# Kernel optimization log

Measured on AMD Instinct MI355X. Metric: run time of the kernel, lower is better.

## Reference

```python
import jax, jax.numpy as jnp
import numpy as np

B, S, DIN, E, H, L, F, DOUT = 16, 1024, 64, 512, 8, 6, 2048, 2
DH = E // H
EPS = 1e-5

def _make_pe(n, d):
    # replicates PositionalEncoding buffer: pe[pos, 2i]=sin, pe[pos,2i+1]=cos
    pos = np.arange(n, dtype=np.float32)[:, None]
    div = np.exp(np.arange(0, d, 2, dtype=np.float32) * (-np.log(10000.0) / d))
    pe = np.zeros((n, d), dtype=np.float32)
    pe[:, 0::2] = np.sin(pos * div)
    pe[:, 1::2] = np.cos(pos * div)
    return pe

def _layernorm(x, g, b):
    m = jnp.mean(x, axis=-1, keepdims=True)
    v = jnp.mean((x - m) ** 2, axis=-1, keepdims=True)
    return (x - m) * jax.lax.rsqrt(v + EPS) * g + b

def setup_inputs() -> dict:
    key = jax.random.key(0)
    ks = iter(jax.random.split(key, 40))
    def xavier(k, shape):
        fan_in, fan_out = shape[-2], shape[-1]
        lim = np.sqrt(6.0 / (fan_in + fan_out)).astype(np.float32)
        return jax.random.uniform(k, shape, jnp.float32, -lim, lim)
    inp = {}
    inp['x'] = jax.random.normal(next(ks), (B, S, DIN), jnp.float32)
    inp['Win'] = xavier(next(ks), (DIN, E)); inp['b_in'] = jnp.zeros((E,), jnp.float32)
    # pe[:x.size(0)] with batch-first x -> slice first B positions, broadcast over seq
    inp['pe'] = jnp.asarray(_make_pe(B, E))[:, None, :]  # [B,1,E]
    inp['Wq'] = xavier(next(ks), (L, E, E)); inp['bq'] = jnp.zeros((L, E), jnp.float32)
    inp['Wk'] = xavier(next(ks), (L, E, E)); inp['bk'] = jnp.zeros((L, E), jnp.float32)
    inp['Wv'] = xavier(next(ks), (L, E, E)); inp['bv'] = jnp.zeros((L, E), jnp.float32)
    inp['Wo'] = xavier(next(ks), (L, E, E)); inp['bo'] = jnp.zeros((L, E), jnp.float32)
    inp['g1'] = jnp.ones((L, E), jnp.float32); inp['be1'] = jnp.zeros((L, E), jnp.float32)
    inp['W1'] = xavier(next(ks), (L, E, F)); inp['b1'] = jnp.zeros((L, F), jnp.float32)
    inp['W2'] = xavier(next(ks), (L, F, E)); inp['b2'] = jnp.zeros((L, E), jnp.float32)
    inp['g2'] = jnp.ones((L, E), jnp.float32); inp['be2'] = jnp.zeros((L, E), jnp.float32)
    inp['gf'] = jnp.ones((E,), jnp.float32); inp['bef'] = jnp.zeros((E,), jnp.float32)
    inp['Wout'] = xavier(next(ks), (E, DOUT)); inp['bout'] = jnp.zeros((DOUT,), jnp.float32)
    return inp

def reference(x, Win, b_in, pe, Wq, bq, Wk, bk, Wv, bv, Wo, bo,
              g1, be1, W1, b1, W2, b2, g2, be2, gf, bef, Wout, bout):
    scale = 1.0 / np.sqrt(DH).astype(np.float32)
    h = x @ Win + b_in + pe  # [B,S,E], pe broadcast over seq (replicates source bug)
    for i in range(L):
        resid = h
        q = (h @ Wq[i] + bq[i]).reshape(B, S, H, DH)
        k = (h @ Wk[i] + bk[i]).reshape(B, S, H, DH)
        v = (h @ Wv[i] + bv[i]).reshape(B, S, H, DH)
        scores = jnp.einsum('bqhd,bkhd->bhqk', q, k) * scale
        attn = jax.nn.softmax(scores, axis=-1)
        o = jnp.einsum('bhqk,bkhd->bqhd', attn, v).reshape(B, S, E)
        o = o @ Wo[i] + bo[i]
        a = _layernorm(o + resid, g1[i], be1[i])
        f = jax.nn.relu(a @ W1[i] + b1[i]) @ W2[i] + b2[i]
        h = _layernorm(f + a, g2[i], be2[i])
    out = _layernorm(h, gf, bef) @ Wout + bout
    return out
```

## Files before the change

kernel.cpp:

```cpp
#include <hip/hip_runtime.h>
#include <hip/hip_bf16.h>

typedef __bf16 bf16_t;
typedef __bf16 bf16x8 __attribute__((ext_vector_type(8)));
typedef __bf16 bf16x4 __attribute__((ext_vector_type(4)));
typedef float f32x4 __attribute__((ext_vector_type(4)));

#define B_ 16
#define S_ 1024
#define E_ 512
#define H_ 8
#define DH_ 64
#define L_ 6
#define F_ 2048
#define M_ (B_ * S_)

#define EXP2F(x) __builtin_amdgcn_exp2f(x)

#define GLOAD_LDS16(gsrc, ldst) \
    __builtin_amdgcn_global_load_lds((const __attribute__((address_space(1))) void*)(gsrc), \
                                     (__attribute__((address_space(3))) void*)(ldst), 16, 0, 0)

__global__ void cast_bf16_kernel(const float* __restrict__ src, bf16_t* __restrict__ dst, int n) {
    int i = (blockIdx.x * 256 + threadIdx.x) * 4;
    if (i + 3 < n) {
        f32x4 v = *(const f32x4*)&src[i];
        #pragma unroll
        for (int j = 0; j < 4; ++j) dst[i + j] = (bf16_t)v[j];
    }
}

__global__ void castT_kernel(const float* __restrict__ src, bf16_t* __restrict__ dst,
                             int K, int N, size_t dstZ) {
    __shared__ bf16_t tile[32][33];
    size_t so = (size_t)blockIdx.z * K * N;
    size_t dofs = (size_t)blockIdx.z * dstZ;
    int k0 = blockIdx.y * 32, n0 = blockIdx.x * 32;
    int tx = threadIdx.x, ty = threadIdx.y;
    for (int i = ty; i < 32; i += 8)
        tile[i][tx] = (bf16_t)src[so + (size_t)(k0 + i) * N + n0 + tx];
    __syncthreads();
    for (int i = ty; i < 32; i += 8)
        dst[dofs + (size_t)(n0 + i) * K + k0 + tx] = tile[tx][i];
}

__global__ void pack_bias_kernel(const float* __restrict__ bq, const float* __restrict__ bk,
                                 const float* __restrict__ bv, float* __restrict__ dst) {
    int i = blockIdx.x * 256 + threadIdx.x;
    if (i >= L_ * 1536) return;
    int l = i / 1536, c = i % 1536;
    float v = (c < 512) ? bq[l * 512 + c] : (c < 1024 ? bk[l * 512 + c - 512] : bv[l * 512 + c - 1024]);
    dst[i] = v;
}

template<int EPI, bool RELU>
__launch_bounds__(256, 2)
__global__ void gemm_kernel(const bf16_t* __restrict__ A, const bf16_t* __restrict__ BT,
                            const float* __restrict__ bias, bf16_t* __restrict__ out16,
                            const float* __restrict__ auxf,
                            int M, int N, int K)
{
    __shared__ bf16_t As[2][128][32];
    __shared__ bf16_t Bs[2][128][32];
    const int tid = threadIdx.x;
    const int lane = tid & 63;
    const int w = tid >> 6;
    const int wm = w >> 1, wn = w & 1;
    const int m0 = blockIdx.x * 128, n0 = blockIdx.y * 128;
    const int l15 = lane & 15, lg = lane >> 4;

    const int srow = w * 32 + (lane >> 2);
    const int scol = (lane & 3) * 8;
    const bf16_t* Ab = A + (size_t)(m0 + srow) * K + scol;
    const bf16_t* Bb = BT + (size_t)(n0 + srow) * K + scol;

    f32x4 acc[4][4] = {};
    const int nt = K >> 5;

    #define STAGE(buf, t) do { \
        size_t ko_ = (size_t)(t) * 32; \
        _Pragma("unroll") \
        for (int j_ = 0; j_ < 2; ++j_) { \
            GLOAD_LDS16(Ab + (size_t)j_ * 16 * K + ko_, &As[buf][w * 32 + j_ * 16][0]); \
            GLOAD_LDS16(Bb + (size_t)j_ * 16 * K + ko_, &Bs[buf][w * 32 + j_ * 16][0]); \
        } } while (0)

    STAGE(0, 0);
    __syncthreads();
    int cur = 0;
    for (int t = 0; t < nt; ++t) {
        if (t + 1 < nt) STAGE(cur ^ 1, t + 1);
        bf16x8 af[4], bfr[4];
        #pragma unroll
        for (int m = 0; m < 4; ++m) af[m] = *(const bf16x8*)&As[cur][wm * 64 + m * 16 + l15][lg * 8];
        #pragma unroll
        for (int n = 0; n < 4; ++n) bfr[n] = *(const bf16x8*)&Bs[cur][wn * 64 + n * 16 + l15][lg * 8];
        __builtin_amdgcn_s_setprio(1);
        #pragma unroll
        for (int m = 0; m < 4; ++m)
            #pragma unroll
            for (int n = 0; n < 4; ++n)
                acc[m][n] = __builtin_amdgcn_mfma_f32_16x16x32_bf16(af[m], bfr[n], acc[m][n], 0, 0, 0);
        __builtin_amdgcn_s_setprio(0);
        __syncthreads();
        cur ^= 1;
    }
    #undef STAGE

    #pragma unroll
    for (int m = 0; m < 4; ++m) {
        #pragma unroll
        for (int n = 0; n < 4; ++n) {
            int col = n0 + wn * 64 + n * 16 + l15;
            float bv = bias[col];
            #pragma unroll
            for (int r = 0; r < 4; ++r) {
                int row = m0 + wm * 64 + m * 16 + lg * 4 + r;
                float v = acc[m][n][r] + bv;
                if (EPI == 1) v += auxf[(size_t)(row >> 10) * E_ + col];
                if (RELU) v = fmaxf(v, 0.f);
                out16[(size_t)row * N + col] = (bf16_t)v;
            }
        }
    }
}

template<int EPI, bool RELU>
__launch_bounds__(512, 2)
__global__ void gemm2_kernel(const bf16_t* __restrict__ A, const bf16_t* __restrict__ BT,
                             const float* __restrict__ bias, bf16_t* __restrict__ out16,
                             const bf16_t* __restrict__ auxb,
                             bf16_t* __restrict__ outk, bf16_t* __restrict__ outv,
                             int M, int N, int K)
{
    __shared__ bf16_t AB[4][12288];
    const int tid = threadIdx.x;
    const int lane = tid & 63;
    const int w = tid >> 6;
    const int wr = w >> 2, wc = w & 3;
    const int m0 = blockIdx.x * 128, n0 = blockIdx.y * 256;
    const int l15 = lane & 15, lg = lane >> 4;

    const int srow = w * 16 + (lane >> 2);
    const int scol = ((lane & 3) ^ ((lane >> 3) & 3)) * 8;
    const int cswz = (lg ^ ((l15 >> 1) & 3)) * 8;
    const bf16_t* Ab  = A  + (size_t)(m0 + srow) * K + scol;
    const bf16_t* Bb0 = BT + (size_t)(n0 + srow) * K + scol;
    const bf16_t* Bb1 = BT + (size_t)(n0 + 128 + srow) * K + scol;

    f32x4 acc[4][4] = {};
    const int nt = K >> 5;

    #define STAGE3(kt, buf) do { \
        size_t ko_ = (size_t)(kt) * 32; \
        GLOAD_LDS16(Ab  + ko_, &AB[buf][w * 512]); \
        GLOAD_LDS16(Bb0 + ko_, &AB[buf][4096 + w * 512]); \
        GLOAD_LDS16(Bb1 + ko_, &AB[buf][8192 + w * 512]); \
    } while (0)

    STAGE3(0, 0);
    STAGE3(1, 1);
    asm volatile("s_waitcnt vmcnt(3)" ::: "memory");
    __builtin_amdgcn_s_barrier();

    int t = 0;
    for (; t + 2 < nt; ++t) {
        const int cur = t & 3;
        bf16x8 af[4], bf[4];
        #pragma unroll
        for (int m = 0; m < 4; ++m)
            af[m] = *(const bf16x8*)&AB[cur][(wr * 64 + m * 16 + l15) * 32 + cswz];
        #pragma unroll
        for (int n = 0; n < 4; ++n)
            bf[n] = *(const bf16x8*)&AB[cur][4096 + (wc * 64 + n * 16 + l15) * 32 + cswz];
        STAGE3(t + 2, (t + 2) & 3);
        asm volatile("s_waitcnt vmcnt(3)" ::: "memory");
        __builtin_amdgcn_s_barrier();
        __builtin_amdgcn_s_setprio(1);
        #pragma unroll
        for (int m = 0; m < 4; ++m)
            #pragma unroll
            for (int n = 0; n < 4; ++n)
                acc[m][n] = __builtin_amdgcn_mfma_f32_16x16x32_bf16(af[m], bf[n], acc[m][n], 0, 0, 0);
        __builtin_amdgcn_s_setprio(0);
    }
    for (; t < nt; ++t) {
        const int cur = t & 3;
        bf16x8 af[4], bf[4];
        #pragma unroll
        for (int m = 0; m < 4; ++m)
            af[m] = *(const bf16x8*)&AB[cur][(wr * 64 + m * 16 + l15) * 32 + cswz];
        #pragma unroll
        for (int n = 0; n < 4; ++n)
            bf[n] = *(const bf16x8*)&AB[cur][4096 + (wc * 64 + n * 16 + l15) * 32 + cswz];
        asm volatile("s_waitcnt vmcnt(0)" ::: "memory");
        __builtin_amdgcn_s_barrier();
        __builtin_amdgcn_s_setprio(1);
        #pragma unroll
        for (int m = 0; m < 4; ++m)
            #pragma unroll
            for (int n = 0; n < 4; ++n)
                acc[m][n] = __builtin_amdgcn_mfma_f32_16x16x32_bf16(af[m], bf[n], acc[m][n], 0, 0, 0);
        __builtin_amdgcn_s_setprio(0);
    }
    #undef STAGE3

    #pragma unroll
    for (int m = 0; m < 4; ++m) {
        #pragma unroll
        for (int n = 0; n < 4; ++n) {
            int col = n0 + wc * 64 + n * 16 + l15;
            float bv = bias[col];
            if (EPI == 4 && col >= 1024) {
                int row0 = m0 + wr * 64 + m * 16 + lg * 4;
                int b = row0 >> 10, s0 = row0 & 1023;
                int vcol = col - 1024;
                bf16x4 pk;
                #pragma unroll
                for (int r = 0; r < 4; ++r) pk[r] = (bf16_t)(acc[m][n][r] + bv);
                *(bf16x4*)&outv[((size_t)(b * H_ + (vcol >> 6)) * DH_ + (vcol & 63)) * S_ + s0] = pk;
            } else {
                #pragma unroll
                for (int r = 0; r < 4; ++r) {
                    int row = m0 + wr * 64 + m * 16 + lg * 4 + r;
                    float v = acc[m][n][r] + bv;
                    if (EPI == 0) {
                        if (RELU) v = fmaxf(v, 0.f);
                        out16[(size_t)row * N + col] = (bf16_t)v;
                    } else if (EPI == 2) {
                        v += (float)auxb[(size_t)row * N + col];
                        out16[(size_t)row * N + col] = (bf16_t)v;
                    } else {
                        if (col < 512) out16[(size_t)row * 512 + col] = (bf16_t)v;
                        else           outk[(size_t)row * 512 + (col - 512)] = (bf16_t)v;
                    }
                }
            }
        }
    }
}

__launch_bounds__(512, 4)
__global__ void attn_kernel(const bf16_t* __restrict__ q, const bf16_t* __restrict__ k,
                            const bf16_t* __restrict__ vt, bf16_t* __restrict__ o)
{
    const int id = blockIdx.x;
    const int rest = id >> 3;
    const int qb = rest & 3;
    const int bh = (id & 7) * 16 + (rest >> 2);
    const int b = bh >> 3, h = bh & 7;
    const int tid = threadIdx.x, lane = tid & 63, w = tid >> 6;
    const int l15 = lane & 15, lg = lane >> 4;
    const int q0 = qb * 256 + w * 32;

    __shared__ bf16_t Ks[2][64 * 64];
    __shared__ bf16_t Vs[2][64 * 64];
    __shared__ char psh_all[8][4096];
    char* psh = psh_all[w];
    const int swz = (l15 & 7) << 4;

    const bf16_t* kb = k + (size_t)b * S_ * E_ + h * DH_;
    const bf16_t* vb = vt + (size_t)(b * H_ + h) * DH_ * S_;

    const int r8 = lane >> 3, c8 = lane & 7;

    #define STAGE_ATTN(buf, kk0) do { \
        int row_ = w * 8 + r8; \
        int ch_ = (c8 ^ r8) * 8; \
        GLOAD_LDS16(kb + (size_t)((kk0) + row_) * E_ + ch_, &Ks[buf][(w * 8) * 64]); \
        GLOAD_LDS16(vb + (size_t)row_ * S_ + (kk0) + ch_, &Vs[buf][(w * 8) * 64]); \
    } while (0)

    bf16x8 aq[2][2];
    #pragma unroll
    for (int m = 0; m < 2; ++m) {
        const size_t qoff = (size_t)(b * S_ + q0 + m * 16 + l15) * E_ + h * DH_;
        aq[m][0] = *(const bf16x8*)&q[qoff + lg * 8];
        aq[m][1] = *(const bf16x8*)&q[qoff + 32 + lg * 8];
    }

    float lrow[2] = {0.f, 0.f};
    f32x4 accO[2][4] = {};

    const float sc = 0.125f * 1.44269504f;
    const int c0 = (lg ^ (l15 & 7)) * 8;
    const int c1 = c0 ^ 32;

    STAGE_ATTN(0, 0);
    __syncthreads();
    int cur = 0;

    for (int it = 0; it < S_ / 64; ++it) {
        if (it + 1 < S_ / 64) STAGE_ATTN(cur ^ 1, (it + 1) * 64);

        f32x4 sf[2][4];
        #pragma unroll
        for (int n = 0; n < 4; ++n) {
            const int r = n * 16 + l15;
            bf16x8 bk0 = *(const bf16x8*)&Ks[cur][r * 64 + c0];
            bf16x8 bk1 = *(const bf16x8*)&Ks[cur][r * 64 + c1];
            __builtin_amdgcn_s_setprio(1);
            #pragma unroll
            for (int m = 0; m < 2; ++m) {
                f32x4 s = {};
                s = __builtin_amdgcn_mfma_f32_16x16x32_bf16(bk0, aq[m][0], s, 0, 0, 0);
                s = __builtin_amdgcn_mfma_f32_16x16x32_bf16(bk1, aq[m][1], s, 0, 0, 0);
                sf[m][n] = s;
            }
            __builtin_amdgcn_s_setprio(0);
        }

        #pragma unroll
        for (int m = 0; m < 2; ++m) {
            float ps = 0.f;
            #pragma unroll
            for (int n = 0; n < 4; ++n) {
                bf16x4 pw;
                #pragma unroll
                for (int r = 0; r < 4; ++r) {
                    float pv = EXP2F(fmaf(sf[m][n][r], sc, -16.f));
                    ps += pv;
                    pw[r] = (bf16_t)pv;
                }
                *(bf16x4*)(psh + (m * 16 + l15) * 128 + ((n * 32 + lg * 8) ^ swz)) = pw;
            }
            ps += __shfl_xor(ps, 16, 64);
            ps += __shfl_xor(ps, 32, 64);
            lrow[m] += ps;
        }
        asm volatile("" ::: "memory");

        bf16x8 pa[2][2];
        #pragma unroll
        for (int m = 0; m < 2; ++m)
            #pragma unroll
            for (int kk = 0; kk < 2; ++kk)
                pa[m][kk] = *(const bf16x8*)(psh + (m * 16 + l15) * 128 + ((kk * 64 + lg * 16) ^ swz));
        bf16x8 vv[4];
        #pragma unroll
        for (int dt = 0; dt < 4; ++dt)
            vv[dt] = *(const bf16x8*)&Vs[cur][(dt * 16 + l15) * 64 + c0];
        __builtin_amdgcn_s_setprio(1);
        #pragma unroll
        for (int dt = 0; dt < 4; ++dt)
            #pragma unroll
            for (int m = 0; m < 2; ++m)
                accO[m][dt] = __builtin_amdgcn_mfma_f32_16x16x32_bf16(vv[dt], pa[m][0], accO[m][dt], 0, 0, 0);
        __builtin_amdgcn_s_setprio(0);
        #pragma unroll
        for (int dt = 0; dt < 4; ++dt)
            vv[dt] = *(const bf16x8*)&Vs[cur][(dt * 16 + l15) * 64 + c1];
        __builtin_amdgcn_s_setprio(1);
        #pragma unroll
        for (int dt = 0; dt < 4; ++dt)
            #pragma unroll
            for (int m = 0; m < 2; ++m)
                accO[m][dt] = __builtin_amdgcn_mfma_f32_16x16x32_bf16(vv[dt], pa[m][1], accO[m][dt], 0, 0, 0);
        __builtin_amdgcn_s_setprio(0);

        __syncthreads();
        cur ^= 1;
    }
    #undef STAGE_ATTN

    #pragma unroll
    for (int m = 0; m < 2; ++m) {
        float rl = 1.f / lrow[m];
        #pragma unroll
        for (int dt = 0; dt < 4; ++dt) {
            bf16x4 ov;
            #pragma unroll
            for (int r = 0; r < 4; ++r) ov[r] = (bf16_t)(accO[m][dt][r] * rl);
            *(bf16x4*)&o[(size_t)(b * S_ + q0 + m * 16 + l15) * E_ + h * DH_ + dt * 16 + lg * 4] = ov;
        }
    }
}

__launch_bounds__(256)
__global__ void ln_kernel(const bf16_t* __restrict__ in, const float* __restrict__ g,
                          const float* __restrict__ be, bf16_t* __restrict__ out)
{
    int row = blockIdx.x * 4 + (threadIdx.x >> 6);
    int lane = threadIdx.x & 63;
    bf16x8 v = *(const bf16x8*)&in[(size_t)row * E_ + lane * 8];
    float x[8];
    #pragma unroll
    for (int j = 0; j < 8; ++j) x[j] = (float)v[j];
    float s = 0.f;
    #pragma unroll
    for (int j = 0; j < 8; ++j) s += x[j];
    #pragma unroll
    for (int off = 32; off >= 1; off >>= 1) s += __shfl_xor(s, off, 64);
    float mean = s * (1.f / E_);
    float vs = 0.f;
    #pragma unroll
    for (int j = 0; j < 8; ++j) { float d = x[j] - mean; vs += d * d; }
    #pragma unroll
    for (int off = 32; off >= 1; off >>= 1) vs += __shfl_xor(vs, off, 64);
    float rstd = rsqrtf(vs * (1.f / E_) + 1e-5f);
    bf16x8 y;
    #pragma unroll
    for (int j = 0; j < 8; ++j) {
        int col = lane * 8 + j;
        y[j] = (bf16_t)((x[j] - mean) * rstd * g[col] + be[col]);
    }
    *(bf16x8*)&out[(size_t)row * E_ + lane * 8] = y;
}

__launch_bounds__(256)
__global__ void final_kernel(const bf16_t* __restrict__ in, const float* __restrict__ g,
                             const float* __restrict__ be, const float* __restrict__ Wout,
                             const float* __restrict__ bout, float* __restrict__ out)
{
    int row = blockIdx.x * 4 + (threadIdx.x >> 6);
    int lane = threadIdx.x & 63;
    bf16x8 v = *(const bf16x8*)&in[(size_t)row * E_ + lane * 8];
    float x[8];
    #pragma unroll
    for (int j = 0; j < 8; ++j) x[j] = (float)v[j];
    float s = 0.f;
    #pragma unroll
    for (int j = 0; j < 8; ++j) s += x[j];
    #pragma unroll
    for (int off = 32; off >= 1; off >>= 1) s += __shfl_xor(s, off, 64);
    float mean = s * (1.f / E_);
    float vs = 0.f;
    #pragma unroll
    for (int j = 0; j < 8; ++j) { float d = x[j] - mean; vs += d * d; }
    #pragma unroll
    for (int off = 32; off >= 1; off >>= 1) vs += __shfl_xor(vs, off, 64);
    float rstd = rsqrtf(vs * (1.f / E_) + 1e-5f);
    float p0 = 0.f, p1 = 0.f;
    #pragma unroll
    for (int j = 0; j < 8; ++j) {
        int col = lane * 8 + j;
        float y = (x[j] - mean) * rstd * g[col] + be[col];
        p0 += y * Wout[col * 2 + 0];
        p1 += y * Wout[col * 2 + 1];
    }
    #pragma unroll
    for (int off = 32; off >= 1; off >>= 1) { p0 += __shfl_xor(p0, off, 64); p1 += __shfl_xor(p1, off, 64); }
    if (lane == 0) {
        out[(size_t)row * 2 + 0] = p0 + bout[0];
        out[(size_t)row * 2 + 1] = p1 + bout[1];
    }
}

extern "C" void kernel_launch(void* const* d_in, const int* in_sizes, int n_in,
                              void* d_out, int out_size, void* d_ws, size_t ws_size,
                              hipStream_t stream)
{
    (void)in_sizes; (void)n_in; (void)out_size;
    const float* x    = (const float*)d_in[0];
    const float* Win  = (const float*)d_in[1];
    const float* b_in = (const float*)d_in[2];
    const float* pe   = (const float*)d_in[3];
    const float* Wq   = (const float*)d_in[4];
    const float* bq   = (const float*)d_in[5];
    const float* Wk   = (const float*)d_in[6];
    const float* bk   = (const float*)d_in[7];
    const float* Wv   = (const float*)d_in[8];
    const float* bv   = (const float*)d_in[9];
    const float* Wo   = (const float*)d_in[10];
    const float* bo   = (const float*)d_in[11];
    const float* g1   = (const float*)d_in[12];
    const float* be1  = (const float*)d_in[13];
    const float* W1   = (const float*)d_in[14];
    const float* b1   = (const float*)d_in[15];
    const float* W2   = (const float*)d_in[16];
    const float* b2   = (const float*)d_in[17];
    const float* g2   = (const float*)d_in[18];
    const float* be2  = (const float*)d_in[19];
    const float* gf   = (const float*)d_in[20];
    const float* bef  = (const float*)d_in[21];
    const float* Wout = (const float*)d_in[22];
    const float* bout = (const float*)d_in[23];

    char* p = (char*)d_ws;
    auto take = [&](size_t bytes) { char* r = p; p += (bytes + 255) & ~(size_t)255; return r; };

    bf16_t* xb    = (bf16_t*)take((size_t)M_ * 64 * 2);
    bf16_t* WinT  = (bf16_t*)take((size_t)E_ * 64 * 2);
    bf16_t* WqkvT = (bf16_t*)take((size_t)L_ * 1536 * E_ * 2);
    bf16_t* WoT   = (bf16_t*)take((size_t)L_ * E_ * E_ * 2);
    bf16_t* W1T   = (bf16_t*)take((size_t)L_ * E_ * F_ * 2);
    bf16_t* W2T   = (bf16_t*)take((size_t)L_ * E_ * F_ * 2);
    float*  bqkv  = (float*)take((size_t)L_ * 1536 * 4);
    bf16_t* hb16  = (bf16_t*)take((size_t)M_ * E_ * 2);
    bf16_t* qb16  = (bf16_t*)take((size_t)M_ * E_ * 2);
    bf16_t* kb16  = (bf16_t*)take((size_t)M_ * E_ * 2);
    bf16_t* vtb   = (bf16_t*)take((size_t)M_ * E_ * 2);
    bf16_t* ob16  = (bf16_t*)take((size_t)M_ * E_ * 2);
    bf16_t* tb16  = (bf16_t*)take((size_t)M_ * E_ * 2);
    bf16_t* ab16  = (bf16_t*)take((size_t)M_ * E_ * 2);
    bf16_t* f1b   = qb16;

    if ((size_t)(p - (char*)d_ws) > ws_size) return;

    cast_bf16_kernel<<<dim3(M_ * 64 / 4 / 256), dim3(256), 0, stream>>>(x, xb, M_ * 64);
    castT_kernel<<<dim3(E_ / 32, 64 / 32, 1), dim3(32, 8), 0, stream>>>(Win, WinT, 64, E_, 0);
    castT_kernel<<<dim3(E_ / 32, E_ / 32, L_), dim3(32, 8), 0, stream>>>(
        Wq, WqkvT + (size_t)0 * E_, E_, E_, (size_t)1536 * E_);
    castT_kernel<<<dim3(E_ / 32, E_ / 32, L_), dim3(32, 8), 0, stream>>>(
        Wk, WqkvT + (size_t)512 * E_, E_, E_, (size_t)1536 * E_);
    castT_kernel<<<dim3(E_ / 32, E_ / 32, L_), dim3(32, 8), 0, stream>>>(
        Wv, WqkvT + (size_t)1024 * E_, E_, E_, (size_t)1536 * E_);
    castT_kernel<<<dim3(E_ / 32, E_ / 32, L_), dim3(32, 8), 0, stream>>>(
        Wo, WoT, E_, E_, (size_t)E_ * E_);
    castT_kernel<<<dim3(F_ / 32, E_ / 32, L_), dim3(32, 8), 0, stream>>>(
        W1, W1T, E_, F_, (size_t)E_ * F_);
    castT_kernel<<<dim3(E_ / 32, F_ / 32, L_), dim3(32, 8), 0, stream>>>(
        W2, W2T, F_, E_, (size_t)E_ * F_);
    pack_bias_kernel<<<dim3((L_ * 1536 + 255) / 256), dim3(256), 0, stream>>>(bq, bk, bv, bqkv);

    gemm_kernel<1, false><<<dim3(M_ / 128, E_ / 128), dim3(256), 0, stream>>>(
        xb, WinT, b_in, hb16, pe, M_, E_, 64);

    for (int i = 0; i < L_; ++i) {
        const bf16_t* WqkvTi = WqkvT + (size_t)i * 1536 * E_;
        const bf16_t* WoTi   = WoT + (size_t)i * E_ * E_;
        const bf16_t* W1Ti   = W1T + (size_t)i * E_ * F_;
        const bf16_t* W2Ti   = W2T + (size_t)i * E_ * F_;

        gemm2_kernel<4, false><<<dim3(M_ / 128, 1536 / 256), dim3(512), 0, stream>>>(
            hb16, WqkvTi, bqkv + (size_t)i * 1536, qb16, nullptr, kb16, vtb, M_, 1536, E_);
        attn_kernel<<<dim3(512), dim3(512), 0, stream>>>(qb16, kb16, vtb, ob16);
        gemm2_kernel<2, false><<<dim3(M_ / 128, E_ / 256), dim3(512), 0, stream>>>(
            ob16, WoTi, bo + i * E_, tb16, hb16, nullptr, nullptr, M_, E_, E_);
        ln_kernel<<<dim3(M_ / 4), dim3(256), 0, stream>>>(tb16, g1 + i * E_, be1 + i * E_, ab16);
        gemm2_kernel<0, true><<<dim3(M_ / 128, F_ / 256), dim3(512), 0, stream>>>(
            ab16, W1Ti, b1 + i * F_, f1b, nullptr, nullptr, nullptr, M_, F_, E_);
        gemm2_kernel<2, false><<<dim3(M_ / 128, E_ / 256), dim3(512), 0, stream>>>(
            f1b, W2Ti, b2 + i * E_, tb16, ab16, nullptr, nullptr, M_, E_, F_);
        ln_kernel<<<dim3(M_ / 4), dim3(256), 0, stream>>>(tb16, g2 + i * E_, be2 + i * E_, hb16);
    }

    final_kernel<<<dim3(M_ / 4), dim3(256), 0, stream>>>(hb16, gf, bef, Wout, bout, (float*)d_out);
}
```

Baseline: 1.245 ms.

## Fuse residual add and LayerNorm into full-row output-projection and FFN2 GEMMs

Adds a gemm3 kernel in which each block computes a 64x512 output tile covering whole rows, using a 3-stage LDS pipeline. Bias, residual add and LayerNorm are then applied in the epilogue, with row statistics reduced across waves through shared memory. This replaces the Wo and W2 GEMMs plus the two separate ln_kernel launches and drops the fp32-free temporary buffer round trip through HBM. The trade-off is fewer blocks (256) at one block per CU, a smaller M tile, and a single-pass E[x^2]-mean^2 variance that is numerically less robust.

```diff
diff --git a/kernel.cpp b/kernel.cpp
--- a/kernel.cpp
+++ b/kernel.cpp
@@ -129,7 +129,6 @@
 __launch_bounds__(512, 2)
 __global__ void gemm2_kernel(const bf16_t* __restrict__ A, const bf16_t* __restrict__ BT,
                              const float* __restrict__ bias, bf16_t* __restrict__ out16,
-                             const bf16_t* __restrict__ auxb,
                              bf16_t* __restrict__ outk, bf16_t* __restrict__ outv,
                              int M, int N, int K)
 {
@@ -227,14 +226,148 @@
                     if (EPI == 0) {
                         if (RELU) v = fmaxf(v, 0.f);
                         out16[(size_t)row * N + col] = (bf16_t)v;
-                    } else if (EPI == 2) {
-                        v += (float)auxb[(size_t)row * N + col];
-                        out16[(size_t)row * N + col] = (bf16_t)v;
                     } else {
                         if (col < 512) out16[(size_t)row * 512 + col] = (bf16_t)v;
                         else           outk[(size_t)row * 512 + (col - 512)] = (bf16_t)v;
                     }
                 }
+            }
+        }
+    }
+}
+
+__launch_bounds__(512, 1)
+__global__ void gemm3_kernel(const bf16_t* __restrict__ A, const bf16_t* __restrict__ BT,
+                             const float* __restrict__ bias, const bf16_t* __restrict__ resid,
+                             const float* __restrict__ g, const float* __restrict__ be,
+                             bf16_t* __restrict__ out, int K)
+{
+    __shared__ bf16_t KV[3][18432];
+    __shared__ float stats[64][4][2];
+    const int tid = threadIdx.x;
+    const int lane = tid & 63;
+    const int w = tid >> 6;
+    const int wr = w >> 2, wc = w & 3;
+    const int m0 = blockIdx.x * 64;
+    const int l15 = lane & 15, lg = lane >> 4;
+
+    const int scol = ((lane & 3) ^ ((lane >> 3) & 3)) * 8;
+    const int cswz = (lg ^ ((l15 >> 1) & 3)) * 8;
+    const int lrow = lane >> 2;
+    const bf16_t* Asrc = A + (size_t)(m0 + (w & 3) * 16 + lrow) * K + scol;
+    const bf16_t* Bsrc[4];
+    #pragma unroll
+    for (int j = 0; j < 4; ++j)
+        Bsrc[j] = BT + (size_t)(w * 64 + j * 16 + lrow) * K + scol;
+
+    f32x4 acc[2][8] = {};
+    const int nt = K >> 5;
+
+    #define STAGE_G3(kt, buf) do { \
+        size_t ko_ = (size_t)(kt) * 32; \
+        _Pragma("unroll") \
+        for (int j_ = 0; j_ < 4; ++j_) \
+            GLOAD_LDS16(Bsrc[j_] + ko_, &KV[buf][2048 + (w * 64 + j_ * 16) * 32]); \
+        GLOAD_LDS16(Asrc + ko_, &KV[buf][((w & 3) * 16) * 32]); \
+    } while (0)
+
+    STAGE_G3(0, 0);
+    STAGE_G3(1, 1);
+    asm volatile("s_waitcnt vmcnt(5)" ::: "memory");
+    __builtin_amdgcn_s_barrier();
+
+    int t = 0, bc = 0, bs = 2;
+    for (; t + 2 < nt; ++t) {
+        bf16x8 af[2], bf[8];
+        #pragma unroll
+        for (int m = 0; m < 2; ++m)
+            af[m] = *(const bf16x8*)&KV[bc][(wr * 32 + m * 16 + l15) * 32 + cswz];
+        #pragma unroll
+        for (int n = 0; n < 8; ++n)
+            bf[n] = *(const bf16x8*)&KV[bc][2048 + (wc * 128 + n * 16 + l15) * 32 + cswz];
+        STAGE_G3(t + 2, bs);
+        asm volatile("s_waitcnt vmcnt(5)" ::: "memory");
+        __builtin_amdgcn_s_barrier();
+        __builtin_amdgcn_s_setprio(1);
+        #pragma unroll
+        for (int m = 0; m < 2; ++m)
+            #pragma unroll
+            for (int n = 0; n < 8; ++n)
+                acc[m][n] = __builtin_amdgcn_mfma_f32_16x16x32_bf16(af[m], bf[n], acc[m][n], 0, 0, 0);
+        __builtin_amdgcn_s_setprio(0);
+        bc = (bc == 2) ? 0 : bc + 1;
+        bs = (bs == 2) ? 0 : bs + 1;
+    }
+    for (; t < nt; ++t) {
+        bf16x8 af[2], bf[8];
+        #pragma unroll
+        for (int m = 0; m < 2; ++m)
+            af[m] = *(const bf16x8*)&KV[bc][(wr * 32 + m * 16 + l15) * 32 + cswz];
+        #pragma unroll
+        for (int n = 0; n < 8; ++n)
+            bf[n] = *(const bf16x8*)&KV[bc][2048 + (wc * 128 + n * 16 + l15) * 32 + cswz];
+        asm volatile("s_waitcnt vmcnt(0)" ::: "memory");
+        __builtin_amdgcn_s_barrier();
+        __builtin_amdgcn_s_setprio(1);
+        #pragma unroll
+        for (int m = 0; m < 2; ++m)
+            #pragma unroll
+            for (int n = 0; n < 8; ++n)
+                acc[m][n] = __builtin_amdgcn_mfma_f32_16x16x32_bf16(af[m], bf[n], acc[m][n], 0, 0, 0);
+        __builtin_amdgcn_s_setprio(0);
+        bc = (bc == 2) ? 0 : bc + 1;
+    }
+    #undef STAGE_G3
+
+    #pragma unroll
+    for (int m = 0; m < 2; ++m) {
+        float ps = 0.f, pq = 0.f;
+        #pragma unroll
+        for (int n = 0; n < 8; ++n) {
+            int col = wc * 128 + n * 16 + l15;
+            float bv = bias[col];
+            #pragma unroll
+            for (int r = 0; r < 4; ++r) {
+                int row = m0 + wr * 32 + m * 16 + lg * 4 + r;
+                float v = acc[m][n][r] + bv + (float)resid[(size_t)row * 512 + col];
+                acc[m][n][r] = v;
+            }
+        }
+        #pragma unroll
+        for (int r = 0; r < 4; ++r) {
+            float s = 0.f, q = 0.f;
+            #pragma unroll
+            for (int n = 0; n < 8; ++n) { float v = acc[m][n][r]; s += v; q += v * v; }
+            #pragma unroll
+            for (int off = 8; off >= 1; off >>= 1) {
+                s += __shfl_xor(s, off, 64);
+                q += __shfl_xor(q, off, 64);
+            }
+            if (l15 == 0) {
+                int rowl = wr * 32 + m * 16 + lg * 4 + r;
+                stats[rowl][wc][0] = s;
+                stats[rowl][wc][1] = q;
+            }
+        }
+        (void)ps; (void)pq;
+    }
+    __syncthreads();
+
+    #pragma unroll
+    for (int m = 0; m < 2; ++m) {
+        #pragma unroll
+        for (int r = 0; r < 4; ++r) {
+            int rowl = wr * 32 + m * 16 + lg * 4 + r;
+            float s = stats[rowl][0][0] + stats[rowl][1][0] + stats[rowl][2][0] + stats[rowl][3][0];
+            float q = stats[rowl][0][1] + stats[rowl][1][1] + stats[rowl][2][1] + stats[rowl][3][1];
+            float mean = s * (1.f / 512.f);
+            float var = q * (1.f / 512.f) - mean * mean;
+            float rstd = rsqrtf(var + 1e-5f);
+            #pragma unroll
+            for (int n = 0; n < 8; ++n) {
+                int col = wc * 128 + n * 16 + l15;
+                float y = (acc[m][n][r] - mean) * rstd * g[col] + be[col];
+                out[(size_t)(m0 + rowl) * 512 + col] = (bf16_t)y;
             }
         }
     }
@@ -374,37 +507,6 @@
             *(bf16x4*)&o[(size_t)(b * S_ + q0 + m * 16 + l15) * E_ + h * DH_ + dt * 16 + lg * 4] = ov;
         }
     }
-}
-
-__launch_bounds__(256)
-__global__ void ln_kernel(const bf16_t* __restrict__ in, const float* __restrict__ g,
-                          const float* __restrict__ be, bf16_t* __restrict__ out)
-{
-    int row = blockIdx.x * 4 + (threadIdx.x >> 6);
-    int lane = threadIdx.x & 63;
-    bf16x8 v = *(const bf16x8*)&in[(size_t)row * E_ + lane * 8];
-    float x[8];
-    #pragma unroll
-    for (int j = 0; j < 8; ++j) x[j] = (float)v[j];
-    float s = 0.f;
-    #pragma unroll
-    for (int j = 0; j < 8; ++j) s += x[j];
-    #pragma unroll
-    for (int off = 32; off >= 1; off >>= 1) s += __shfl_xor(s, off, 64);
-    float mean = s * (1.f / E_);
-    float vs = 0.f;
-    #pragma unroll
-    for (int j = 0; j < 8; ++j) { float d = x[j] - mean; vs += d * d; }
-    #pragma unroll
-    for (int off = 32; off >= 1; off >>= 1) vs += __shfl_xor(vs, off, 64);
-    float rstd = rsqrtf(vs * (1.f / E_) + 1e-5f);
-    bf16x8 y;
-    #pragma unroll
-    for (int j = 0; j < 8; ++j) {
-        int col = lane * 8 + j;
-        y[j] = (bf16_t)((x[j] - mean) * rstd * g[col] + be[col]);
-    }
-    *(bf16x8*)&out[(size_t)row * E_ + lane * 8] = y;
 }
 
 __launch_bounds__(256)
@@ -491,7 +593,6 @@
     bf16_t* kb16  = (bf16_t*)take((size_t)M_ * E_ * 2);
     bf16_t* vtb   = (bf16_t*)take((size_t)M_ * E_ * 2);
     bf16_t* ob16  = (bf16_t*)take((size_t)M_ * E_ * 2);
-    bf16_t* tb16  = (bf16_t*)take((size_t)M_ * E_ * 2);
     bf16_t* ab16  = (bf16_t*)take((size_t)M_ * E_ * 2);
     bf16_t* f1b   = qb16;
 
@@ -523,16 +624,14 @@
         const bf16_t* W2Ti   = W2T + (size_t)i * E_ * F_;
 
         gemm2_kernel<4, false><<<dim3(M_ / 128, 1536 / 256), dim3(512), 0, stream>>>(
-            hb16, WqkvTi, bqkv + (size_t)i * 1536, qb16, nullptr, kb16, vtb, M_, 1536, E_);
+            hb16, WqkvTi, bqkv + (size_t)i * 1536, qb16, kb16, vtb, M_, 1536, E_);
         attn_kernel<<<dim3(512), dim3(512), 0, stream>>>(qb16, kb16, vtb, ob16);
-        gemm2_kernel<2, false><<<dim3(M_ / 128, E_ / 256), dim3(512), 0, stream>>>(
-            ob16, WoTi, bo + i * E_, tb16, hb16, nullptr, nullptr, M_, E_, E_);
-        ln_kernel<<<dim3(M_ / 4), dim3(256), 0, stream>>>(tb16, g1 + i * E_, be1 + i * E_, ab16);
+        gemm3_kernel<<<dim3(M_ / 64), dim3(512), 0, stream>>>(
+            ob16, WoTi, bo + i * E_, hb16, g1 + i * E_, be1 + i * E_, ab16, E_);
         gemm2_kernel<0, true><<<dim3(M_ / 128, F_ / 256), dim3(512), 0, stream>>>(
-            ab16, W1Ti, b1 + i * F_, f1b, nullptr, nullptr, nullptr, M_, F_, E_);
-        gemm2_kernel<2, false><<<dim3(M_ / 128, E_ / 256), dim3(512), 0, stream>>>(
-            f1b, W2Ti, b2 + i * E_, tb16, ab16, nullptr, nullptr, M_, E_, F_);
-        ln_kernel<<<dim3(M_ / 4), dim3(256), 0, stream>>>(tb16, g2 + i * E_, be2 + i * E_, hb16);
+            ab16, W1Ti, b1 + i * F_, f1b, nullptr, nullptr, M_, F_, E_);
+        gemm3_kernel<<<dim3(M_ / 64), dim3(512), 0, stream>>>(
+            f1b, W2Ti, b2 + i * E_, ab16, g2 + i * E_, be2 + i * E_, hb16, F_);
     }
 
     final_kernel<<<dim3(M_ / 4), dim3(256), 0, stream>>>(hb16, gf, bef, Wout, bout, (float*)d_out);
```

New measurement: 1.293 ms. +3.9%, slower.
